# Kernel tuning notes

Measured on AMD Instinct MI355X. Metric: run time of the kernel, lower is better.

Reference implementation:

```python
import jax, jax.numpy as jnp
import numpy as np
from jax import lax

B, CIN, HF, WF = 8, 512, 60, 60      # encoder feature
NCLS = 19                            # seg out channels
PATCH = 10                           # patch_size
DEPTH = 8                            # 2**att_depth
UPS = 8                              # seg upsampling
HI = HF * UPS                        # 480 upsampled image size
NP_IMG = (HI // PATCH) ** 2          # 2304 image patches
NP_FEA = (HI // DEPTH // PATCH) ** 2 # 36 feature patches
POOL_SIZES = (1, 2, 3, 6)


def resize_ac(x, H, W):
    # bilinear, align_corners=True (matches F.interpolate/UpsamplingBilinear2d)
    b, c, h, w = x.shape
    ys = jnp.arange(H, dtype=x.dtype) * ((h - 1) / max(H - 1, 1))
    xs = jnp.arange(W, dtype=x.dtype) * ((w - 1) / max(W - 1, 1))
    y0 = jnp.floor(ys).astype(jnp.int32); y1 = jnp.minimum(y0 + 1, h - 1)
    x0 = jnp.floor(xs).astype(jnp.int32); x1 = jnp.minimum(x0 + 1, w - 1)
    wy = (ys - y0.astype(x.dtype))[:, None]
    wx = (xs - x0.astype(x.dtype))[None, :]
    g = lambda yi, xi: x[:, :, yi[:, None], xi[None, :]]
    top = (1 - wx) * g(y0, x0) + wx * g(y0, x1)
    bot = (1 - wx) * g(y1, x0) + wx * g(y1, x1)
    return (1 - wy) * top + wy * bot


def bn_eval(x, gamma, beta, mean, var, eps=1e-5):
    s = lambda v: v[None, :, None, None]
    return (x - s(mean)) * (s(gamma) / jnp.sqrt(s(var) + eps)) + s(beta)


def setup_inputs() -> dict:
    key = jax.random.key(0)
    ks = jax.random.split(key, 16)
    f32 = jnp.float32
    return {
        "feat": jax.random.normal(ks[0], (B, CIN, HF, WF), f32),
        "attentions": jax.random.normal(ks[1], (B, NCLS, NP_IMG, NP_FEA), f32),
        "w_psp": jax.random.normal(ks[2], (4, CIN // 4, CIN), f32) * 0.03,
        "b_psp0": jax.random.normal(ks[3], (CIN // 4,), f32) * 0.02,
        "bn_psp_gamma": jax.random.uniform(ks[4], (3, CIN // 4), f32, 0.5, 1.5),
        "bn_psp_beta": jax.random.normal(ks[5], (3, CIN // 4), f32) * 0.02,
        "bn_psp_mean": jax.random.normal(ks[6], (3, CIN // 4), f32) * 0.02,
        "bn_psp_var": jax.random.uniform(ks[7], (3, CIN // 4), f32, 0.5, 1.5),
        "w_conv": jax.random.normal(ks[8], (512, 2 * CIN), f32) * 0.03,
        "bn_conv_gamma": jax.random.uniform(ks[9], (512,), f32, 0.5, 1.5),
        "bn_conv_beta": jax.random.normal(ks[10], (512,), f32) * 0.02,
        "bn_conv_mean": jax.random.normal(ks[11], (512,), f32) * 0.02,
        "bn_conv_var": jax.random.uniform(ks[12], (512,), f32, 0.5, 1.5),
        "w_segconv": jax.random.normal(ks[13], (NCLS, 512, 3, 3), f32) * 0.03,
        "b_segconv": jax.random.normal(ks[14], (NCLS,), f32) * 0.02,
    }


def _forward(feat, attentions, w_psp, b_psp0, bn_psp_gamma, bn_psp_beta,
             bn_psp_mean, bn_psp_var, w_conv, bn_conv_gamma, bn_conv_beta,
             bn_conv_mean, bn_conv_var, w_segconv, b_segconv):
    # ---- PSP pyramid ----
    branches = []
    for i, p in enumerate(POOL_SIZES):
        k = HF // p
        pooled = feat.reshape(B, CIN, p, k, p, k).mean(axis=(3, 5))  # adaptive avg pool
        y = jnp.einsum('oc,bchw->bohw', w_psp[i], pooled)
        if i == 0:  # pool_size==1 -> no BN, conv has bias
            y = y + b_psp0[None, :, None, None]
        else:
            y = bn_eval(y, bn_psp_gamma[i-1], bn_psp_beta[i-1],
                        bn_psp_mean[i-1], bn_psp_var[i-1])
        y = jax.nn.relu(y)
        branches.append(resize_ac(y, HF, WF))
    x = jnp.concatenate(branches + [feat], axis=1)  # [B, 2*CIN, HF, WF]

    # ---- 1x1 Conv2dReLU + BN (eval), dropout is identity in eval ----
    x = jnp.einsum('oc,bchw->bohw', w_conv, x)
    x = jax.nn.relu(bn_eval(x, bn_conv_gamma, bn_conv_beta, bn_conv_mean, bn_conv_var))

    # ---- SegmentationHead ----
    x = lax.conv_general_dilated(x, w_segconv, (1, 1), 'SAME',
                                 dimension_numbers=('NCHW', 'OIHW', 'NCHW'))
    x = x + b_segconv[None, :, None, None]
    x = resize_ac(x, HI, HI)  # [B, NCLS, 480, 480]

    # one-hot of per-pixel argmax (scatter of ones)
    am = jnp.argmax(x, axis=1)
    x_softmax = (am[:, None] == jnp.arange(NCLS)[None, :, None, None]).astype(x.dtype)

    # grouped ones-conv stride 8 / 64 == 8x8 average pooling
    hf = HI // DEPTH  # 60
    argx_feamap = x_softmax.reshape(B, NCLS, hf, DEPTH, hf, DEPTH).mean(axis=(3, 5))

    # unfold(k=10, s=10): [B, C, 36, 100] (blocks row-major, patch row-major)
    nb = hf // PATCH  # 6
    unf = argx_feamap.reshape(B, NCLS, nb, PATCH, nb, PATCH)
    unf = unf.transpose(0, 1, 2, 4, 3, 5).reshape(B, NCLS, nb * nb, PATCH * PATCH)

    counts = jnp.count_nonzero(attentions, axis=-1, keepdims=True).astype(x.dtype) + 1e-5
    att = jnp.einsum('bcpk,bckq->bcpq', attentions / counts, unf)  # [B,C,2304,100]

    # fold back to [B, C, 480, 480]
    nbi = HI // PATCH  # 48
    corr = att.reshape(B, NCLS, nbi, nbi, PATCH, PATCH)
    corr = corr.transpose(0, 1, 2, 4, 3, 5).reshape(B, NCLS, HI, HI)

    x = corr * x + x  # activation=None -> identity
    return x, attentions


def reference(feat, attentions, w_psp, b_psp0, bn_psp_gamma, bn_psp_beta,
              bn_psp_mean, bn_psp_var, w_conv, bn_conv_gamma, bn_conv_beta,
              bn_conv_mean, bn_conv_var, w_segconv, b_segconv):
    return _forward(feat, attentions, w_psp, b_psp0, bn_psp_gamma, bn_psp_beta,
                    bn_psp_mean, bn_psp_var, w_conv, bn_conv_gamma, bn_conv_beta,
                    bn_conv_mean, bn_conv_var, w_segconv, b_segconv)
```

## Files before the change

### kernel.cpp

```cpp
#include <hip/hip_runtime.h>
#include <stdint.h>

#define NB 8
#define NCLS 19

typedef short s8v __attribute__((ext_vector_type(8)));
typedef float f4v __attribute__((ext_vector_type(4)));

__device__ __forceinline__ unsigned short f2b(float f){
  union { float f; uint32_t u; } v; v.f = f;
  uint32_t u = v.u;
  uint32_t r = (u + 0x7fffu + ((u >> 16) & 1u)) >> 16;
  return (unsigned short)r;
}

#define GLOAD16(g, l) __builtin_amdgcn_global_load_lds( \
    (const __attribute__((address_space(1))) unsigned int*)(g), \
    (__attribute__((address_space(3))) unsigned int*)(l), 16, 0, 0)

#define OFF_X512 0
#define OFF_POOL 31490048
#define OFF_Z    32309248
#define OFF_BNS  33128448
#define OFF_BNB  33130496
#define OFF_SEG  33132544
#define OFF_ARGX 35321344
#define OFF_WSEG 37510144
#define OFF_WF   37805056

__global__ __launch_bounds__(256) void k_setup(
    const float* __restrict__ feat, unsigned short* __restrict__ featT,
    unsigned short* __restrict__ x512p,
    const float* __restrict__ wseg, unsigned short* __restrict__ wsegT,
    const float* __restrict__ wconv, unsigned short* __restrict__ wfT,
    const float* __restrict__ g, const float* __restrict__ be,
    const float* __restrict__ m, const float* __restrict__ v,
    float* __restrict__ sc, float* __restrict__ sh,
    unsigned short* __restrict__ argxT)
{
  __shared__ unsigned short lt[64*528];
  int bid = blockIdx.x;
  if (bid < 456){
    int b = bid / 57, px0 = (bid - b*57)*64;
    for (int i = threadIdx.x; i < 64*512; i += 256){
      int c = i >> 6, px = i & 63;
      float val = feat[((size_t)b*512 + c)*3600 + min(px0+px, 3599)];
      lt[px*528 + c] = f2b(val);
    }
    __syncthreads();
    for (int i = threadIdx.x; i < 4096; i += 256){
      int px = i >> 6, c8 = i & 63;
      s8v vv = *(const s8v*)(lt + px*528 + c8*8);
      *(s8v*)(featT + ((size_t)b*3712 + px0 + px)*512 + c8*8) = vv;
    }
    return;
  }
  bid -= 456;
  if (bid < 488){
    int idx = bid*256 + threadIdx.x;
    if (idx < 124928){
      int pix = idx >> 6;
      int ch  = (idx & 63) << 3;
      int b = pix / 244;
      int r = pix - b*244;
      int h, w;
      if (r < 62){ h = 0; w = r; }
      else if (r < 124){ h = 61; w = r - 62; }
      else if (r < 184){ h = r - 124 + 1; w = 0; }
      else { h = r - 184 + 1; w = 61; }
      s8v z = (s8v){0,0,0,0,0,0,0,0};
      *(s8v*)(x512p + (((size_t)b*62 + h)*62 + w)*512 + ch) = z;
    }
    return;
  }
  bid -= 488;
  if (bid < 576){
    int idx = bid*256 + threadIdx.x;
    if (idx < 9*32*512){
      int tap = idx / (32*512);
      int rem = idx - tap*(32*512);
      int o = rem >> 9, c = rem & 511;
      float val = (o < NCLS) ? wseg[((size_t)o*512 + c)*9 + tap] : 0.0f;
      wsegT[idx] = f2b(val);
    }
    return;
  }
  bid -= 576;
  if (bid < 1024){
    int idx = bid*256 + threadIdx.x;
    if (idx < 512*512){
      int o = idx >> 9, c = idx & 511;
      wfT[idx] = f2b(wconv[(size_t)o*1024 + 512 + c]);
    }
    return;
  }
  bid -= 1024;
  if (bid < 2){
    int i = bid*256 + threadIdx.x;
    if (i < 512){
      float s = g[i] * rsqrtf(v[i] + 1e-5f);
      sc[i] = s; sh[i] = be[i] - m[i]*s;
    }
    return;
  }
  bid -= 2;
  {
    int gi = bid*256 + threadIdx.x;
    if (gi < 136192){
      s8v z = (s8v){0,0,0,0,0,0,0,0};
      ((s8v*)argxT)[gi] = z;
    }
  }
}

__global__ __launch_bounds__(64) void k1_pool(const float* __restrict__ feat, float* __restrict__ pooled){
  int bc = blockIdx.x;
  __shared__ float rs[64][12];
  int r = threadIdx.x;
  if (r < 60){
    const float* row = feat + (size_t)bc*3600 + r*60;
    float s6[6];
    #pragma unroll
    for (int j = 0; j < 6; j++){
      float s = 0.f;
      #pragma unroll
      for (int i = 0; i < 10; i++) s += row[j*10+i];
      s6[j] = s;
    }
    float s3_0 = s6[0]+s6[1], s3_1 = s6[2]+s6[3], s3_2 = s6[4]+s6[5];
    float s2_0 = s3_0 + s6[2], s2_1 = s6[3] + s3_2;
    rs[r][0]  = s2_0 + s2_1;
    rs[r][1]  = s2_0; rs[r][2]  = s2_1;
    rs[r][3]  = s3_0; rs[r][4]  = s3_1; rs[r][5] = s3_2;
    #pragma unroll
    for (int j = 0; j < 6; j++) rs[r][6+j] = s6[j];
  }
  __syncthreads();
  int t = threadIdx.x;
  if (t < 50){
    int P, by, bx, jcol;
    if (t == 0){ P=1; by=0; bx=0; jcol=0; }
    else if (t < 5){ P=2; int l=t-1; by=l>>1; bx=l&1; jcol=1+bx; }
    else if (t < 14){ P=3; int l=t-5; by=l/3; bx=l-(l/3)*3; jcol=3+bx; }
    else { P=6; int l=t-14; by=l/6; bx=l-(l/6)*6; jcol=6+bx; }
    int k = 60/P;
    float s = 0.f;
    for (int rr = 0; rr < k; rr++) s += rs[by*k+rr][jcol];
    pooled[(size_t)bc*50 + t] = s * (1.0f/((float)k*(float)k));
  }
}

__global__ __launch_bounds__(256) void k2_branch(
    const float* __restrict__ pooled, const float* __restrict__ w_psp,
    const float* __restrict__ b_psp0,
    const float* __restrict__ png, const float* __restrict__ pnb,
    const float* __restrict__ pnm, const float* __restrict__ pnv,
    const float* __restrict__ wconv, float* __restrict__ zbuf)
{
  int bin = blockIdx.x % 50;
  int b   = blockIdx.x / 50;
  int br  = (bin < 1) ? 0 : (bin < 5) ? 1 : (bin < 14) ? 2 : 3;
  __shared__ float pl[512];
  __shared__ float ysh[128];
  int t = threadIdx.x;
  pl[t]       = pooled[((size_t)b*512 + t)*50 + bin];
  pl[t + 256] = pooled[((size_t)b*512 + t + 256)*50 + bin];
  __syncthreads();
  if (t < 128){
    const float* wr = w_psp + ((size_t)br*128 + t)*512;
    float s = 0.f;
    #pragma unroll 8
    for (int c = 0; c < 512; c++) s += pl[c]*wr[c];
    if (br == 0) s += b_psp0[t];
    else {
      int ib = (br-1)*128 + t;
      s = (s - pnm[ib]) * png[ib] * rsqrtf(pnv[ib] + 1e-5f) + pnb[ib];
    }
    ysh[t] = fmaxf(s, 0.f);
  }
  __syncthreads();
  for (int o = t; o < 512; o += 256){
    const float* wc = wconv + (size_t)o*1024 + br*128;
    float s = 0.f;
    #pragma unroll
    for (int c = 0; c < 128; c++) s += ysh[c]*wc[c];
    zbuf[((size_t)b*50 + bin)*512 + o] = s;
  }
}

__global__ __launch_bounds__(256) void k3_gemm(
    const unsigned short* __restrict__ featT, const unsigned short* __restrict__ wfT,
    const float* __restrict__ zbuf, const float* __restrict__ bns,
    const float* __restrict__ bnb, unsigned short* __restrict__ x512p)
{
  __shared__ unsigned short lmem[2*128*64];
  unsigned short* lA = lmem;
  unsigned short* lB = lmem + 128*64;

  const int t = threadIdx.x;
  const int lane = t & 63;
  const int wave = t >> 6;
  const int wm = wave >> 1;
  const int wn = wave & 1;
  const int pix0 = blockIdx.x * 128;
  const int o0   = blockIdx.y * 128;
  const int b    = blockIdx.z;

  f4v acc[4][4];
  #pragma unroll
  for (int i = 0; i < 4; i++)
    #pragma unroll
    for (int j = 0; j < 4; j++)
      acc[i][j] = (f4v){0.f,0.f,0.f,0.f};

  const int sub  = lane >> 3;
  const int slot = lane & 7;

  for (int kk = 0; kk < 8; kk++){
    #pragma unroll
    for (int j = 0; j < 4; j++){
      int px = j*32 + wave*8 + sub;
      int pix = min(pix0 + px, 3599);
      const unsigned short* src = featT + ((size_t)b*3712 + pix)*512 + kk*64 + ((slot ^ (px & 7)) << 3);
      GLOAD16(src, lA + j*2048 + wave*512);
    }
    #pragma unroll
    for (int j = 0; j < 4; j++){
      int o = j*32 + wave*8 + sub;
      const unsigned short* src = wfT + (size_t)(o0 + o)*512 + kk*64 + ((slot ^ (o & 7)) << 3);
      GLOAD16(src, lB + j*2048 + wave*512);
    }
    __syncthreads();
    #pragma unroll
    for (int ks = 0; ks < 2; ks++){
      const int chunk = ks*4 + (lane >> 4);
      s8v af[4], bg[4];
      #pragma unroll
      for (int mf = 0; mf < 4; mf++){
        int p = wm*64 + mf*16 + (lane & 15);
        af[mf] = *(s8v*)((char*)lA + p*128 + ((chunk ^ (p & 7)))*16);
      }
      #pragma unroll
      for (int nf = 0; nf < 4; nf++){
        int o = wn*64 + nf*16 + (lane & 15);
        bg[nf] = *(s8v*)((char*)lB + o*128 + ((chunk ^ (o & 7)))*16);
      }
      #pragma unroll
      for (int mf = 0; mf < 4; mf++)
        #pragma unroll
        for (int nf = 0; nf < 4; nf++)
          acc[mf][nf] = __builtin_amdgcn_mfma_f32_16x16x32_bf16(af[mf], bg[nf], acc[mf][nf], 0, 0, 0);
    }
    __syncthreads();
  }

  float* zl  = (float*)lmem;
  float* lsc = zl + 50*128;
  float* lsh = lsc + 128;
  for (int i = t; i < 50*128; i += 256){
    int bin = i >> 7, ol = i & 127;
    zl[i] = zbuf[((size_t)b*50 + bin)*512 + o0 + ol];
  }
  if (t < 128){ lsc[t] = bns[o0 + t]; lsh[t] = bnb[o0 + t]; }
  __syncthreads();

  #pragma unroll
  for (int mf = 0; mf < 4; mf++){
    #pragma unroll
    for (int r = 0; r < 4; r++){
      int p = pix0 + wm*64 + mf*16 + (lane >> 4)*4 + r;
      if (p >= 3600) continue;
      int h = p / 60, w = p - (p/60)*60;
      float wgt[3][4]; int bix[3][4];
      const int pbase[3] = {1,5,14};
      const int psz[3]   = {2,3,6};
      #pragma unroll
      for (int ib = 0; ib < 3; ib++){
        int P = psz[ib];
        float fy = (float)h * (float)(P-1) / 59.0f;
        float fx = (float)w * (float)(P-1) / 59.0f;
        int y0 = (int)fy; int y1 = min(y0+1, P-1); float wy = fy - (float)y0;
        int x0 = (int)fx; int x1 = min(x0+1, P-1); float wx = fx - (float)x0;
        bix[ib][0] = pbase[ib] + y0*P + x0; wgt[ib][0] = (1.f-wy)*(1.f-wx);
        bix[ib][1] = pbase[ib] + y0*P + x1; wgt[ib][1] = (1.f-wy)*wx;
        bix[ib][2] = pbase[ib] + y1*P + x0; wgt[ib][2] = wy*(1.f-wx);
        bix[ib][3] = pbase[ib] + y1*P + x1; wgt[ib][3] = wy*wx;
      }
      size_t obase = (((size_t)b*62 + (h+1))*62 + (w+1))*512 + o0;
      #pragma unroll
      for (int nf = 0; nf < 4; nf++){
        int ol = wn*64 + nf*16 + (lane & 15);
        float zs = zl[ol];
        #pragma unroll
        for (int ib = 0; ib < 3; ib++)
          #pragma unroll
          for (int tp = 0; tp < 4; tp++)
            zs += wgt[ib][tp] * zl[bix[ib][tp]*128 + ol];
        float v = acc[mf][nf][r] + zs;
        v = fmaxf(v * lsc[ol] + lsh[ol], 0.f);
        x512p[obase + ol] = f2b(v);
      }
    }
  }
}

__global__ __launch_bounds__(256) void k4_conv(
    const unsigned short* __restrict__ x512p, const unsigned short* __restrict__ wsegT,
    const float* __restrict__ bseg, float* __restrict__ seg60)
{
  __shared__ unsigned short lW[32*512];
  const int h = blockIdx.x;
  const int b = blockIdx.y;
  const int t = threadIdx.x;
  const int lane = t & 63;
  const int wave = t >> 6;
  const int wpix = wave*16 + (lane & 15);
  const int wld = min(wpix, 59);

  f4v acc[2];
  acc[0] = (f4v){0.f,0.f,0.f,0.f};
  acc[1] = (f4v){0.f,0.f,0.f,0.f};

  for (int tap = 0; tap < 9; tap++){
    __syncthreads();
    for (int i = t; i < 2048; i += 256){
      int orow = i >> 6;
      int cn = i & 63;
      s8v v = *(const s8v*)(wsegT + ((size_t)tap*32 + orow)*512 + cn*8);
      *(s8v*)((char*)lW + orow*1024 + ((cn ^ (orow & 7)))*16) = v;
    }
    __syncthreads();
    int dy = tap/3 - 1, dx = tap - (tap/3)*3 - 1;
    const unsigned short* arow = x512p + (((size_t)b*62 + (h+dy+1))*62 + (wld+dx+1))*512 + (lane>>4)*8;
    #pragma unroll 4
    for (int cs = 0; cs < 16; cs++){
      int cb = cs*32;
      s8v a = *(const s8v*)(arow + cb);
      #pragma unroll
      for (int nf = 0; nf < 2; nf++){
        int o = nf*16 + (lane & 15);
        int chunk = (cb >> 3) + (lane >> 4);
        s8v bv = *(s8v*)((char*)lW + o*1024 + ((chunk ^ (o & 7)))*16);
        acc[nf] = __builtin_amdgcn_mfma_f32_16x16x32_bf16(a, bv, acc[nf], 0, 0, 0);
      }
    }
  }
  #pragma unroll
  for (int nf = 0; nf < 2; nf++){
    int o = nf*16 + (lane & 15);
    if (o < NCLS){
      float bias = bseg[o];
      #pragma unroll
      for (int r = 0; r < 4; r++){
        int wst = wave*16 + (lane >> 4)*4 + r;
        if (wst < 60)
          seg60[(((size_t)b*60 + h)*60 + wst)*NCLS + o] = acc[nf][r] + bias;
      }
    }
  }
}

__global__ __launch_bounds__(256) void k5_argmax(const float* __restrict__ seg60, unsigned short* __restrict__ argxT){
  int gw = blockIdx.x*4 + (threadIdx.x >> 6);
  int b = gw / 3600;
  int cell = gw - b*3600;
  int fy = cell / 60, fx = cell - (cell/60)*60;
  int lane = threadIdx.x & 63;
  int py = fy*8 + (lane >> 3), px = fx*8 + (lane & 7);
  float yy = (float)py * (59.0f/479.0f); int y0 = (int)yy; int y1 = min(y0+1, 59); float wy = yy - (float)y0;
  float xx = (float)px * (59.0f/479.0f); int x0 = (int)xx; int x1 = min(x0+1, 59); float wx = xx - (float)x0;
  const float* base = seg60 + (size_t)b*3600*NCLS;
  const float* s00 = base + (y0*60 + x0)*NCLS;
  const float* s01 = base + (y0*60 + x1)*NCLS;
  const float* s10 = base + (y1*60 + x0)*NCLS;
  const float* s11 = base + (y1*60 + x1)*NCLS;
  float w00 = (1.f-wy)*(1.f-wx), w01 = (1.f-wy)*wx, w10 = wy*(1.f-wx), w11 = wy*wx;
  float best = -3.0e38f; int bc = 0;
  #pragma unroll
  for (int c = 0; c < NCLS; c++){
    float v = w00*s00[c] + w01*s01[c] + w10*s10[c] + w11*s11[c];
    if (v > best){ best = v; bc = c; }
  }
  int cnt = 0;
  #pragma unroll
  for (int c = 0; c < NCLS; c++){
    unsigned long long m = __ballot(bc == c);
    if (lane == c) cnt = __popcll(m);
  }
  int ky = fy/10, qy = fy - (fy/10)*10, kx = fx/10, qx = fx - (fx/10)*10;
  int q = qy*10 + qx, k = ky*6 + kx;
  if (lane < NCLS){
    unsigned short hv = f2b((float)cnt * (1.0f/64.0f));
    argxT[(size_t)(b*NCLS + lane)*7168 + q*64 + (((k>>3) ^ (q&7))<<3) + (k&7)] = hv;
  }
}

__global__ __launch_bounds__(256) void k7_final(
    const float* __restrict__ att, const unsigned short* __restrict__ argxT,
    const float* __restrict__ seg60, float* __restrict__ out, float* __restrict__ out2)
{
  int pr = blockIdx.x, c = blockIdx.y, b = blockIdx.z;
  __shared__ char pool[22720];
  unsigned short* Abf = (unsigned short*)pool;
  unsigned short* Ubf = (unsigned short*)(pool + 6144);
  float* corrl = (float*)pool;
  float* inv   = (float*)(pool + 21504);
  float* srow  = (float*)(pool + 21696);
  const int t = threadIdx.x;
  const int lane = t & 63;
  const int wave = t >> 6;

  int ybase; { float yy0 = (float)(pr*10)*(59.0f/479.0f); ybase = (int)yy0; }

  const size_t aoff = (((size_t)b*NCLS + c)*2304 + (size_t)pr*48)*36;
  const float* ab = att + aoff;
  float* o2 = out2 + aoff;
  for (int i = t; i < 768; i += 256){
    int pc = i >> 4, j = i & 15;
    ushort4 w4 = make_ushort4(0,0,0,0);
    if (j < 9){
      f4v v = *(const f4v*)(ab + pc*36 + j*4);
      *(f4v*)(o2 + pc*36 + j*4) = v;
      w4.x = f2b(v[0]); w4.y = f2b(v[1]); w4.z = f2b(v[2]); w4.w = f2b(v[3]);
    }
    int ch = j >> 1;
    *(ushort4*)((char*)Abf + pc*128 + (((ch ^ (pc & 7)))<<4) + (j & 1)*8) = w4;
  }
  {
    const unsigned short* up = argxT + (size_t)(b*NCLS + c)*7168;
    #pragma unroll
    for (int r = 0; r < 4; r++){
      int chunk0 = r*256 + wave*64;
      if (chunk0 < 896)
        GLOAD16(up + (size_t)(chunk0 + lane)*8, Ubf + (size_t)chunk0*8);
    }
  }
  if (t < 240){
    int j = t/60, x = t - (t/60)*60;
    int row = min(ybase + j, 59);
    srow[j*64 + x] = seg60[(((size_t)b*60 + row)*60 + x)*NCLS + c];
  }
  if (t < 48){
    int nz = 0;
    #pragma unroll
    for (int j2 = 0; j2 < 9; j2++){
      f4v v = *(const f4v*)(ab + t*36 + j2*4);
      nz += (v[0]!=0.f)+(v[1]!=0.f)+(v[2]!=0.f)+(v[3]!=0.f);
    }
    inv[t] = 1.0f/((float)nz + 1e-5f);
  }
  __syncthreads();

  f4v acc[6];
  #pragma unroll
  for (int s = 0; s < 6; s++) acc[s] = (f4v){0.f,0.f,0.f,0.f};
  #pragma unroll
  for (int s = 0; s < 6; s++){
    int pi = wave + s*4;
    if (pi < 21){
      int M = pi/7, N = pi - (pi/7)*7;
      #pragma unroll
      for (int ks = 0; ks < 2; ks++){
        int chunk = ks*4 + (lane >> 4);
        int ar = M*16 + (lane & 15);
        s8v af = *(s8v*)((char*)Abf + ar*128 + ((chunk ^ (ar & 7))<<4));
        int qr = N*16 + (lane & 15);
        s8v bg = *(s8v*)((char*)Ubf + qr*128 + ((chunk ^ (qr & 7))<<4));
        acc[s] = __builtin_amdgcn_mfma_f32_16x16x32_bf16(af, bg, acc[s], 0, 0, 0);
      }
    }
  }
  float hA[4], hB[4];
  {
    float xxa = (float)t * (59.0f/479.0f);
    int xa0 = (int)xxa; int xa1 = min(xa0+1, 59); float wxa = xxa - (float)xa0;
    int px2 = t + 256;
    float xxb = (float)px2 * (59.0f/479.0f);
    int xb0 = (int)xxb; int xb1 = min(xb0+1, 59); float wxb = xxb - (float)xb0;
    #pragma unroll
    for (int j = 0; j < 4; j++){
      hA[j] = (1.f-wxa)*srow[j*64 + xa0] + wxa*srow[j*64 + xa1];
      hB[j] = (px2 < 480) ? ((1.f-wxb)*srow[j*64 + xb0] + wxb*srow[j*64 + xb1]) : 0.f;
    }
  }
  __syncthreads();

  #pragma unroll
  for (int s = 0; s < 6; s++){
    int pi = wave + s*4;
    if (pi < 21){
      int M = pi/7, N = pi - (pi/7)*7;
      int q = N*16 + (lane & 15);
      #pragma unroll
      for (int r = 0; r < 4; r++){
        int pc = M*16 + (lane >> 4)*4 + r;
        corrl[pc*112 + q] = acc[s][r] * inv[pc];
      }
    }
  }
  __syncthreads();

  float* outb = out + ((size_t)b*NCLS + c)*230400 + (size_t)pr*4800;
  int pcA = (t*6554) >> 16, qxA = t - pcA*10;
  int px2 = t + 256;
  int pcB = (px2*6554) >> 16, qxB = px2 - pcB*10;
  #pragma unroll
  for (int qy = 0; qy < 10; qy++){
    int py = pr*10 + qy;
    float yy = (float)py * (59.0f/479.0f);
    int y0 = (int)yy; int y1 = min(y0+1, 59); float wy = yy - (float)y0;
    int j0 = y0 - ybase, j1 = y1 - ybase;
    float h0a = (j0==0)?hA[0]:(j0==1)?hA[1]:(j0==2)?hA[2]:hA[3];
    float h1a = (j1==0)?hA[0]:(j1==1)?hA[1]:(j1==2)?hA[2]:hA[3];
    float omw = 1.f - wy;
    float xv = omw*h0a + wy*h1a;
    outb[qy*480 + t] = xv * (1.f + corrl[pcA*112 + qy*10 + qxA]);
    if (px2 < 480){
      float h0b = (j0==0)?hB[0]:(j0==1)?hB[1]:(j0==2)?hB[2]:hB[3];
      float h1b = (j1==0)?hB[0]:(j1==1)?hB[1]:(j1==2)?hB[2]:hB[3];
      float xv2 = omw*h0b + wy*h1b;
      outb[qy*480 + px2] = xv2 * (1.f + corrl[pcB*112 + qy*10 + qxB]);
    }
  }
}

extern "C" void kernel_launch(void* const* d_in, const int* in_sizes, int n_in,
                              void* d_out, int out_size, void* d_ws, size_t ws_size,
                              hipStream_t stream)
{
  (void)in_sizes; (void)n_in; (void)out_size; (void)ws_size;
  const float* feat   = (const float*)d_in[0];
  const float* attn   = (const float*)d_in[1];
  const float* w_psp  = (const float*)d_in[2];
  const float* b_psp0 = (const float*)d_in[3];
  const float* png    = (const float*)d_in[4];
  const float* pnb    = (const float*)d_in[5];
  const float* pnm    = (const float*)d_in[6];
  const float* pnv    = (const float*)d_in[7];
  const float* wconv  = (const float*)d_in[8];
  const float* cg     = (const float*)d_in[9];
  const float* cbt    = (const float*)d_in[10];
  const float* cm     = (const float*)d_in[11];
  const float* cv     = (const float*)d_in[12];
  const float* wseg   = (const float*)d_in[13];
  const float* bseg   = (const float*)d_in[14];

  float* out1 = (float*)d_out;
  float* out2 = out1 + (size_t)35020800;

  char* ws = (char*)d_ws;
  unsigned short* x512p = (unsigned short*)(ws + OFF_X512);
  float* pooled = (float*)(ws + OFF_POOL);
  float* zbuf   = (float*)(ws + OFF_Z);
  float* bns    = (float*)(ws + OFF_BNS);
  float* bnb    = (float*)(ws + OFF_BNB);
  float* seg60  = (float*)(ws + OFF_SEG);
  unsigned short* argxT = (unsigned short*)(ws + OFF_ARGX);
  unsigned short* wsegT = (unsigned short*)(ws + OFF_WSEG);
  unsigned short* wfT   = (unsigned short*)(ws + OFF_WF);
  unsigned short* featT = (unsigned short*)d_out;

  k_setup<<<3078, 256, 0, stream>>>(feat, featT, x512p, wseg, wsegT, wconv, wfT,
                                    cg, cbt, cm, cv, bns, bnb, argxT);
  k1_pool<<<4096, 64, 0, stream>>>(feat, pooled);
  k2_branch<<<400, 256, 0, stream>>>(pooled, w_psp, b_psp0, png, pnb, pnm, pnv, wconv, zbuf);
  k3_gemm<<<dim3(29,4,8), 256, 0, stream>>>(featT, wfT, zbuf, bns, bnb, x512p);
  k4_conv<<<dim3(60,8), 256, 0, stream>>>(x512p, wsegT, bseg, seg60);
  k5_argmax<<<7200, 256, 0, stream>>>(seg60, argxT);
  k7_final<<<dim3(48,19,8), 256, 0, stream>>>(attn, argxT, seg60, out1, out2);
}
```

Baseline: 263.8 us.

## Fold pooling into setup kernel and widen GEMM output tile to 256

The standalone pooling kernel is merged into the setup kernel as extra blocks, with four waves per block each handling one channel, which removes one launch. The 1x1-conv GEMM now computes 256 output channels per block instead of 128, so each A tile of features is loaded once and reused across two B tiles, halving A traffic. The cost is double the accumulator registers (128 floats per thread) and 48KB of LDS, which may lower occupancy, and only 464 blocks are launched for the GEMM.

```diff
diff --git a/kernel.cpp b/kernel.cpp
--- a/kernel.cpp
+++ b/kernel.cpp
@@ -36,7 +36,7 @@
     const float* __restrict__ g, const float* __restrict__ be,
     const float* __restrict__ m, const float* __restrict__ v,
     float* __restrict__ sc, float* __restrict__ sh,
-    unsigned short* __restrict__ argxT)
+    unsigned short* __restrict__ argxT, float* __restrict__ pooled)
 {
   __shared__ unsigned short lt[64*528];
   int bid = blockIdx.x;
@@ -104,49 +104,49 @@
     return;
   }
   bid -= 2;
-  {
+  if (bid < 532){
     int gi = bid*256 + threadIdx.x;
     if (gi < 136192){
       s8v z = (s8v){0,0,0,0,0,0,0,0};
       ((s8v*)argxT)[gi] = z;
     }
-  }
-}
-
-__global__ __launch_bounds__(64) void k1_pool(const float* __restrict__ feat, float* __restrict__ pooled){
-  int bc = blockIdx.x;
-  __shared__ float rs[64][12];
-  int r = threadIdx.x;
-  if (r < 60){
-    const float* row = feat + (size_t)bc*3600 + r*60;
-    float s6[6];
-    #pragma unroll
-    for (int j = 0; j < 6; j++){
+    return;
+  }
+  bid -= 532;
+  {
+    int w = threadIdx.x >> 6, lane = threadIdx.x & 63;
+    int bc = bid*4 + w;
+    float* rs = (float*)lt + w*64*12;
+    if (lane < 60){
+      const float* row = feat + (size_t)bc*3600 + lane*60;
+      float s6[6];
+      #pragma unroll
+      for (int j = 0; j < 6; j++){
+        float s = 0.f;
+        #pragma unroll
+        for (int i = 0; i < 10; i++) s += row[j*10+i];
+        s6[j] = s;
+      }
+      float s3_0 = s6[0]+s6[1], s3_1 = s6[2]+s6[3], s3_2 = s6[4]+s6[5];
+      float s2_0 = s3_0 + s6[2], s2_1 = s6[3] + s3_2;
+      rs[lane*12+0] = s2_0 + s2_1;
+      rs[lane*12+1] = s2_0; rs[lane*12+2] = s2_1;
+      rs[lane*12+3] = s3_0; rs[lane*12+4] = s3_1; rs[lane*12+5] = s3_2;
+      #pragma unroll
+      for (int j = 0; j < 6; j++) rs[lane*12+6+j] = s6[j];
+    }
+    __syncthreads();
+    if (lane < 50){
+      int P, by, bx, jcol;
+      if (lane == 0){ P=1; by=0; bx=0; jcol=0; }
+      else if (lane < 5){ P=2; int l=lane-1; by=l>>1; bx=l&1; jcol=1+bx; }
+      else if (lane < 14){ P=3; int l=lane-5; by=l/3; bx=l-(l/3)*3; jcol=3+bx; }
+      else { P=6; int l=lane-14; by=l/6; bx=l-(l/6)*6; jcol=6+bx; }
+      int k = 60/P;
       float s = 0.f;
-      #pragma unroll
-      for (int i = 0; i < 10; i++) s += row[j*10+i];
-      s6[j] = s;
-    }
-    float s3_0 = s6[0]+s6[1], s3_1 = s6[2]+s6[3], s3_2 = s6[4]+s6[5];
-    float s2_0 = s3_0 + s6[2], s2_1 = s6[3] + s3_2;
-    rs[r][0]  = s2_0 + s2_1;
-    rs[r][1]  = s2_0; rs[r][2]  = s2_1;
-    rs[r][3]  = s3_0; rs[r][4]  = s3_1; rs[r][5] = s3_2;
-    #pragma unroll
-    for (int j = 0; j < 6; j++) rs[r][6+j] = s6[j];
-  }
-  __syncthreads();
-  int t = threadIdx.x;
-  if (t < 50){
-    int P, by, bx, jcol;
-    if (t == 0){ P=1; by=0; bx=0; jcol=0; }
-    else if (t < 5){ P=2; int l=t-1; by=l>>1; bx=l&1; jcol=1+bx; }
-    else if (t < 14){ P=3; int l=t-5; by=l/3; bx=l-(l/3)*3; jcol=3+bx; }
-    else { P=6; int l=t-14; by=l/6; bx=l-(l/6)*6; jcol=6+bx; }
-    int k = 60/P;
-    float s = 0.f;
-    for (int rr = 0; rr < k; rr++) s += rs[by*k+rr][jcol];
-    pooled[(size_t)bc*50 + t] = s * (1.0f/((float)k*(float)k));
+      for (int rr = 0; rr < k; rr++) s += rs[(by*k+rr)*12 + jcol];
+      pooled[(size_t)bc*50 + lane] = s * (1.0f/((float)k*(float)k));
+    }
   }
 }
 
@@ -193,9 +193,8 @@
     const float* __restrict__ zbuf, const float* __restrict__ bns,
     const float* __restrict__ bnb, unsigned short* __restrict__ x512p)
 {
-  __shared__ unsigned short lmem[2*128*64];
+  __shared__ unsigned short lmem[3*128*64];
   unsigned short* lA = lmem;
-  unsigned short* lB = lmem + 128*64;
 
   const int t = threadIdx.x;
   const int lane = t & 63;
@@ -203,15 +202,17 @@
   const int wm = wave >> 1;
   const int wn = wave & 1;
   const int pix0 = blockIdx.x * 128;
-  const int o0   = blockIdx.y * 128;
+  const int o0   = blockIdx.y * 256;
   const int b    = blockIdx.z;
 
-  f4v acc[4][4];
-  #pragma unroll
-  for (int i = 0; i < 4; i++)
-    #pragma unroll
-    for (int j = 0; j < 4; j++)
-      acc[i][j] = (f4v){0.f,0.f,0.f,0.f};
+  f4v acc[2][4][4];
+  #pragma unroll
+  for (int oh = 0; oh < 2; oh++)
+    #pragma unroll
+    for (int i = 0; i < 4; i++)
+      #pragma unroll
+      for (int j = 0; j < 4; j++)
+        acc[oh][i][j] = (f4v){0.f,0.f,0.f,0.f};
 
   const int sub  = lane >> 3;
   const int slot = lane & 7;
@@ -225,31 +226,37 @@
       GLOAD16(src, lA + j*2048 + wave*512);
     }
     #pragma unroll
-    for (int j = 0; j < 4; j++){
-      int o = j*32 + wave*8 + sub;
-      const unsigned short* src = wfT + (size_t)(o0 + o)*512 + kk*64 + ((slot ^ (o & 7)) << 3);
-      GLOAD16(src, lB + j*2048 + wave*512);
-    }
+    for (int oh = 0; oh < 2; oh++)
+      #pragma unroll
+      for (int j = 0; j < 4; j++){
+        int o = j*32 + wave*8 + sub;
+        const unsigned short* src = wfT + (size_t)(o0 + oh*128 + o)*512 + kk*64 + ((slot ^ (o & 7)) << 3);
+        GLOAD16(src, lmem + (1+oh)*8192 + j*2048 + wave*512);
+      }
     __syncthreads();
     #pragma unroll
     for (int ks = 0; ks < 2; ks++){
       const int chunk = ks*4 + (lane >> 4);
-      s8v af[4], bg[4];
+      s8v af[4];
       #pragma unroll
       for (int mf = 0; mf < 4; mf++){
         int p = wm*64 + mf*16 + (lane & 15);
         af[mf] = *(s8v*)((char*)lA + p*128 + ((chunk ^ (p & 7)))*16);
       }
       #pragma unroll
-      for (int nf = 0; nf < 4; nf++){
-        int o = wn*64 + nf*16 + (lane & 15);
-        bg[nf] = *(s8v*)((char*)lB + o*128 + ((chunk ^ (o & 7)))*16);
-      }
-      #pragma unroll
-      for (int mf = 0; mf < 4; mf++)
+      for (int oh = 0; oh < 2; oh++){
+        s8v bg[4];
         #pragma unroll
-        for (int nf = 0; nf < 4; nf++)
-          acc[mf][nf] = __builtin_amdgcn_mfma_f32_16x16x32_bf16(af[mf], bg[nf], acc[mf][nf], 0, 0, 0);
+        for (int nf = 0; nf < 4; nf++){
+          int o = wn*64 + nf*16 + (lane & 15);
+          bg[nf] = *(s8v*)((char*)lmem + (1+oh)*16384 + o*128 + ((chunk ^ (o & 7)))*16);
+        }
+        #pragma unroll
+        for (int mf = 0; mf < 4; mf++)
+          #pragma unroll
+          for (int nf = 0; nf < 4; nf++)
+            acc[oh][mf][nf] = __builtin_amdgcn_mfma_f32_16x16x32_bf16(af[mf], bg[nf], acc[oh][mf][nf], 0, 0, 0);
+      }
     }
     __syncthreads();
   }
@@ -257,48 +264,52 @@
   float* zl  = (float*)lmem;
   float* lsc = zl + 50*128;
   float* lsh = lsc + 128;
-  for (int i = t; i < 50*128; i += 256){
-    int bin = i >> 7, ol = i & 127;
-    zl[i] = zbuf[((size_t)b*50 + bin)*512 + o0 + ol];
-  }
-  if (t < 128){ lsc[t] = bns[o0 + t]; lsh[t] = bnb[o0 + t]; }
-  __syncthreads();
-
-  #pragma unroll
-  for (int mf = 0; mf < 4; mf++){
-    #pragma unroll
-    for (int r = 0; r < 4; r++){
-      int p = pix0 + wm*64 + mf*16 + (lane >> 4)*4 + r;
-      if (p >= 3600) continue;
-      int h = p / 60, w = p - (p/60)*60;
-      float wgt[3][4]; int bix[3][4];
-      const int pbase[3] = {1,5,14};
-      const int psz[3]   = {2,3,6};
-      #pragma unroll
-      for (int ib = 0; ib < 3; ib++){
-        int P = psz[ib];
-        float fy = (float)h * (float)(P-1) / 59.0f;
-        float fx = (float)w * (float)(P-1) / 59.0f;
-        int y0 = (int)fy; int y1 = min(y0+1, P-1); float wy = fy - (float)y0;
-        int x0 = (int)fx; int x1 = min(x0+1, P-1); float wx = fx - (float)x0;
-        bix[ib][0] = pbase[ib] + y0*P + x0; wgt[ib][0] = (1.f-wy)*(1.f-wx);
-        bix[ib][1] = pbase[ib] + y0*P + x1; wgt[ib][1] = (1.f-wy)*wx;
-        bix[ib][2] = pbase[ib] + y1*P + x0; wgt[ib][2] = wy*(1.f-wx);
-        bix[ib][3] = pbase[ib] + y1*P + x1; wgt[ib][3] = wy*wx;
-      }
-      size_t obase = (((size_t)b*62 + (h+1))*62 + (w+1))*512 + o0;
-      #pragma unroll
-      for (int nf = 0; nf < 4; nf++){
-        int ol = wn*64 + nf*16 + (lane & 15);
-        float zs = zl[ol];
+  for (int oh = 0; oh < 2; oh++){
+    int o0e = o0 + oh*128;
+    __syncthreads();
+    for (int i = t; i < 50*128; i += 256){
+      int bin = i >> 7, ol = i & 127;
+      zl[i] = zbuf[((size_t)b*50 + bin)*512 + o0e + ol];
+    }
+    if (t < 128){ lsc[t] = bns[o0e + t]; lsh[t] = bnb[o0e + t]; }
+    __syncthreads();
+
+    #pragma unroll
+    for (int mf = 0; mf < 4; mf++){
+      #pragma unroll
+      for (int r = 0; r < 4; r++){
+        int p = pix0 + wm*64 + mf*16 + (lane >> 4)*4 + r;
+        if (p >= 3600) continue;
+        int h = p / 60, w = p - (p/60)*60;
+        float wgt[3][4]; int bix[3][4];
+        const int pbase[3] = {1,5,14};
+        const int psz[3]   = {2,3,6};
         #pragma unroll
-        for (int ib = 0; ib < 3; ib++)
+        for (int ib = 0; ib < 3; ib++){
+          int P = psz[ib];
+          float fy = (float)h * (float)(P-1) / 59.0f;
+          float fx = (float)w * (float)(P-1) / 59.0f;
+          int y0 = (int)fy; int y1 = min(y0+1, P-1); float wy = fy - (float)y0;
+          int x0 = (int)fx; int x1 = min(x0+1, P-1); float wx = fx - (float)x0;
+          bix[ib][0] = pbase[ib] + y0*P + x0; wgt[ib][0] = (1.f-wy)*(1.f-wx);
+          bix[ib][1] = pbase[ib] + y0*P + x1; wgt[ib][1] = (1.f-wy)*wx;
+          bix[ib][2] = pbase[ib] + y1*P + x0; wgt[ib][2] = wy*(1.f-wx);
+          bix[ib][3] = pbase[ib] + y1*P + x1; wgt[ib][3] = wy*wx;
+        }
+        size_t obase = (((size_t)b*62 + (h+1))*62 + (w+1))*512 + o0e;
+        #pragma unroll
+        for (int nf = 0; nf < 4; nf++){
+          int ol = wn*64 + nf*16 + (lane & 15);
+          float zs = zl[ol];
           #pragma unroll
-          for (int tp = 0; tp < 4; tp++)
-            zs += wgt[ib][tp] * zl[bix[ib][tp]*128 + ol];
-        float v = acc[mf][nf][r] + zs;
-        v = fmaxf(v * lsc[ol] + lsh[ol], 0.f);
-        x512p[obase + ol] = f2b(v);
+          for (int ib = 0; ib < 3; ib++)
+            #pragma unroll
+            for (int tp = 0; tp < 4; tp++)
+              zs += wgt[ib][tp] * zl[bix[ib][tp]*128 + ol];
+          float v = acc[oh][mf][nf][r] + zs;
+          v = fmaxf(v * lsc[ol] + lsh[ol], 0.f);
+          x512p[obase + ol] = f2b(v);
+        }
       }
     }
   }
@@ -560,11 +571,10 @@
   unsigned short* wfT   = (unsigned short*)(ws + OFF_WF);
   unsigned short* featT = (unsigned short*)d_out;
 
-  k_setup<<<3078, 256, 0, stream>>>(feat, featT, x512p, wseg, wsegT, wconv, wfT,
-                                    cg, cbt, cm, cv, bns, bnb, argxT);
-  k1_pool<<<4096, 64, 0, stream>>>(feat, pooled);
+  k_setup<<<4102, 256, 0, stream>>>(feat, featT, x512p, wseg, wsegT, wconv, wfT,
+                                    cg, cbt, cm, cv, bns, bnb, argxT, pooled);
   k2_branch<<<400, 256, 0, stream>>>(pooled, w_psp, b_psp0, png, pnb, pnm, pnv, wconv, zbuf);
-  k3_gemm<<<dim3(29,4,8), 256, 0, stream>>>(featT, wfT, zbuf, bns, bnb, x512p);
+  k3_gemm<<<dim3(29,2,8), 256, 0, stream>>>(featT, wfT, zbuf, bns, bnb, x512p);
   k4_conv<<<dim3(60,8), 256, 0, stream>>>(x512p, wsegT, bseg, seg60);
   k5_argmax<<<7200, 256, 0, stream>>>(seg60, argxT);
   k7_final<<<dim3(48,19,8), 256, 0, stream>>>(attn, argxT, seg60, out1, out2);
```

Result: slower. 374.2 us (+41.8%).
